# Kernel tuning notes

Measured on AMD Instinct MI355X. Metric: run time of the kernel, lower is better.

The kernel has to match this reference:

```python
import jax, jax.numpy as jnp
import numpy as np

BLOCK = 64
THRESH = 0.95
EPS = 1e-8


def setup_inputs() -> dict:
    key = jax.random.key(0)
    kq, kk, kv = jax.random.split(key, 3)
    S, D = 4096, 128
    q = jax.random.normal(kq, (S, D), dtype=jnp.float32)
    k = jax.random.normal(kk, (S, D), dtype=jnp.float32)
    v = jax.random.normal(kv, (S, D), dtype=jnp.float32)
    return {"q": q, "k": k, "v": v}


def reference(q, k, v):
    S, D = q.shape
    nb = S // BLOCK
    qb = q.reshape(nb, BLOCK, D)
    kb = k.reshape(nb, BLOCK, D)
    vb = v.reshape(nb, BLOCK, D)
    # all block-pair scores: [nb_q, nb_k, BLOCK_q, BLOCK_k]
    scores = jnp.einsum('ibd,jcd->ijbc', qb, kb)
    m = jnp.max(scores, axis=-1, keepdims=True)
    e = jnp.exp(scores - m)
    s = jnp.sum(e, axis=-1, keepdims=True)  # per-block-pair softmax denominator
    # top-p truncation mask: sort descending, cumsum, threshold
    srt = jnp.sort(e, axis=-1)[..., ::-1]
    cum = jnp.cumsum(srt, axis=-1)
    mask = cum < THRESH * s
    # NOTE: faithful to original — mask (in sorted order) is applied to the
    # UNSORTED exp_scores, exactly as the torch code does (indices unused).
    em = e * mask
    em = em / (jnp.sum(em, axis=-1, keepdims=True) + EPS)
    # accumulate over key blocks j (per-pair normalized weights, summed)
    out = jnp.einsum('ijbc,jcd->ibd', em, vb)
    return out.reshape(S, D)
```

## Files before the change

### kernel.cpp

```cpp
#include <hip/hip_runtime.h>
#include <cstdint>
#include <cstddef>


#define SEQ   4096
#define DIM   128
#define BLK   64
#define NB    (SEQ / BLK)
#define NJG   16
#define JPB   (NB / NJG)
#define NT    256
#define PSTR  12288
#define THRESH 0.95f
#define EPSF   1e-8f
#define PPART  (PSTR * NB)
#define PARTF  (NJG * SEQ * DIM)
#define WS_NEED ((size_t)PPART * 4 + (size_t)PARTF * 4)

typedef __attribute__((ext_vector_type(8))) _Float16 f16x8;
typedef __attribute__((ext_vector_type(4))) float    f32x4;

#define MFMAH(a, b, c) __builtin_amdgcn_mfma_f32_16x16x32_f16((a), (b), (c), 0, 0, 0)

union UH4 { uint2 u; _Float16 h[4]; };
union UH8 { uint4 u; f16x8 v; };

__device__ __forceinline__ void gll16(const uint* g, uint* l) {
  __builtin_amdgcn_global_load_lds(
      (const __attribute__((address_space(1))) void*)g,
      (__attribute__((address_space(3))) void*)l, 16, 0, 0);
}

__global__ __launch_bounds__(NT, 4) void eco_prep_kernel(
    const float* __restrict__ K, const float* __restrict__ V,
    uint* __restrict__ P, float* __restrict__ O) {
  const int tid = threadIdx.x;
  const int w   = blockIdx.x;
  const int jb  = w >> 4;
  const int sub = w & 15;

  if (tid < 128) {
    float4 z = {0.f, 0.f, 0.f, 0.f};
    ((float4*)O)[w * 128 + tid] = z;

    const float4* gk = (const float4*)(K + (size_t)jb * BLK * DIM);
    uint* dst = P + (size_t)jb * PSTR;
    int f = sub * 128 + tid;
    int r = f >> 5, c4 = f & 31;
    float4 x = gk[f];
    float xs[4] = {x.x, x.y, x.z, x.w};
    UH4 uh, ur;
#pragma unroll
    for (int e = 0; e < 4; ++e) {
      float v = xs[e];
      _Float16 h = (_Float16)v;
      uh.h[e] = h;
      ur.h[e] = (_Float16)(v - (float)h);
    }
    uint off = (uint)r * 64u + (((uint)(c4 >> 1) ^ (uint)(r & 15)) << 2) +
               (uint)((c4 & 1) << 1);
    *(uint2*)&dst[off]        = uh.u;
    *(uint2*)&dst[4096 + off] = ur.u;
  } else if (tid < 192) {
    const float* gv = V + (size_t)jb * BLK * DIM;
    uint4* dv = (uint4*)(P + (size_t)jb * PSTR + 8192);
    int idx = sub * 64 + (tid - 128);
    int ch = idx >> 7, d = idx & 127;
    UH8 u;
#pragma unroll
    for (int j = 0; j < 8; ++j)
      u.v[j] = (_Float16)gv[(ch * 8 + j) * DIM + d];
    dv[idx] = u.u;
  }
}

__global__ __launch_bounds__(NT) void eco_reduce_kernel(
    const float* __restrict__ Part, float* __restrict__ O) {
  const int gid = blockIdx.x * NT + threadIdx.x;
  const float4* p4 = (const float4*)Part;
  float4 a = p4[gid];
#pragma unroll
  for (int jg = 1; jg < NJG; ++jg) {
    float4 b = p4[(size_t)jg * (SEQ * DIM / 4) + gid];
    a.x += b.x; a.y += b.y; a.z += b.z; a.w += b.w;
  }
  ((float4*)O)[gid] = a;
}

template <bool PARTIAL>
__global__ __launch_bounds__(NT, 4) void eco_attn_kernel(
    const float* __restrict__ Q, const uint* __restrict__ P,
    float* __restrict__ O, float* __restrict__ Part) {
  __shared__ __align__(16) uint sK[8192];

  const int tid  = threadIdx.x;
  const int ib   = blockIdx.y;
  const int jg   = blockIdx.x;
  const int lane = tid & 63;
  const int wv   = tid >> 6;
  const int quad = lane >> 4;
  const int l16  = lane & 15;
  const int q4   = quad << 2;

  f16x8 qh[4], qr[4];
  {
    const float* qp = Q + (size_t)(ib * BLK + wv * 16 + l16) * DIM + quad * 8;
#pragma unroll
    for (int ks = 0; ks < 4; ++ks) {
      float4 x0 = *(const float4*)(qp + ks * 32);
      float4 x1 = *(const float4*)(qp + ks * 32 + 4);
      float xs[8] = {x0.x, x0.y, x0.z, x0.w, x1.x, x1.y, x1.z, x1.w};
      f16x8 h8, r8;
#pragma unroll
      for (int e = 0; e < 8; ++e) {
        float v = xs[e];
        _Float16 h = (_Float16)v;
        h8[e] = h;
        r8[e] = (_Float16)(v - (float)h);
      }
      qh[ks] = h8; qr[ks] = r8;
    }
  }

  const f32x4 zf = {0.f, 0.f, 0.f, 0.f};
  f32x4 pv[8];
#pragma unroll
  for (int i = 0; i < 8; ++i) pv[i] = zf;

  {
    const uint* gsrc = P + (size_t)(jg * JPB) * PSTR;
#pragma unroll
    for (int it = 0; it < 8; ++it) {
      int idx = (it * NT + tid) << 2;
      gll16(gsrc + idx, sK + idx);
    }
  }

  for (int jj = 0; jj < JPB; ++jj) {
    const int jb = jg * JPB + jj;
    __syncthreads();

    f32x4 acc[4];
#pragma unroll
    for (int nt = 0; nt < 4; ++nt) acc[nt] = zf;
#pragma unroll
    for (int nt = 0; nt < 4; ++nt) {
      const int rB = nt * 16 + l16;
      const uint rowoff = (uint)rB * 64u;
      const uint swk = (uint)(rB & 15);
#pragma unroll
      for (int ks = 0; ks < 4; ++ks) {
        uint off = rowoff + ((((uint)(ks * 4 + quad)) ^ swk) << 2);
        f16x8 bh = *(const f16x8*)&sK[off];
        f16x8 br = *(const f16x8*)&sK[4096 + off];
        acc[nt] = MFMAH(bh, qh[ks], acc[nt]);
        acc[nt] = MFMAH(br, qh[ks], acc[nt]);
        acc[nt] = MFMAH(bh, qr[ks], acc[nt]);
      }
    }
    __syncthreads();

    if (jj + 1 < JPB) {
      const uint* gsrc = P + (size_t)(jb + 1) * PSTR;
#pragma unroll
      for (int it = 0; it < 8; ++it) {
        int idx = (it * NT + tid) << 2;
        gll16(gsrc + idx, sK + idx);
      }
    }

    const uint* gvt = P + (size_t)jb * PSTR + 8192;

    bool doHi;
    uint2 u0, u1, u2, u3;

    {
      float a[16], e[16];
#pragma unroll
      for (int nt = 0; nt < 4; ++nt) {
#pragma unroll
        for (int rg = 0; rg < 4; ++rg) a[nt * 4 + rg] = acc[nt][rg];
      }
      float mt[8];
#pragma unroll
      for (int i = 0; i < 8; ++i) mt[i] = fmaxf(a[i], a[i + 8]);
#pragma unroll
      for (int w2 = 4; w2 >= 1; w2 >>= 1)
#pragma unroll
        for (int i = 0; i < w2; ++i) mt[i] = fmaxf(mt[i], mt[i + w2]);
      float m = mt[0];
      m = fmaxf(m, __shfl_xor(m, 16, 64));
      m = fmaxf(m, __shfl_xor(m, 32, 64));
#pragma unroll
      for (int i = 0; i < 16; ++i) { a[i] = __expf(a[i] - m); e[i] = a[i]; }
      float st[8];
#pragma unroll
      for (int i = 0; i < 8; ++i) st[i] = a[i] + a[i + 8];
#pragma unroll
      for (int w2 = 4; w2 >= 1; w2 >>= 1)
#pragma unroll
        for (int i = 0; i < w2; ++i) st[i] += st[i + w2];
      float sr = st[0];
      sr += __shfl_xor(sr, 16, 64);
      sr += __shfl_xor(sr, 32, 64);
      const float T = THRESH * sr;

      float cum = 1.0f;
      bool live = (cum < T);
      int t = live ? 1 : 0;
#pragma unroll
      for (int i = 0; i < 16; ++i) a[i] = (a[i] >= 1.0f) ? 0.f : a[i];
#pragma unroll
      for (int p4 = 0; p4 < 4; ++p4) {
        float M = fmaxf(fmaxf(fmaxf(a[0], a[1]), a[2]),
                        fmaxf(fmaxf(a[3], a[4]), a[5]));
        M = fmaxf(M, fmaxf(fmaxf(a[6],  a[7]),  a[8]));
        M = fmaxf(M, fmaxf(fmaxf(a[9],  a[10]), a[11]));
        M = fmaxf(M, fmaxf(fmaxf(a[12], a[13]), a[14]));
        M = fmaxf(M, a[15]);
        M = fmaxf(M, __shfl_xor(M, 16, 64));
        M = fmaxf(M, __shfl_xor(M, 32, 64));
        const float cn = cum + M;
        const bool cross = !(cn < T) || !(M > 0.f);
        if (live) { cum = cn; t += cross ? 0 : 1; }
        live = live && !cross;
#pragma unroll
        for (int i = 0; i < 16; ++i) a[i] = (a[i] >= M) ? 0.f : a[i];
      }

      while (__any(live)) {
        float M = fmaxf(fmaxf(fmaxf(a[0], a[1]), a[2]),
                        fmaxf(fmaxf(a[3], a[4]), a[5]));
        M = fmaxf(M, fmaxf(fmaxf(a[6],  a[7]),  a[8]));
        M = fmaxf(M, fmaxf(fmaxf(a[9],  a[10]), a[11]));
        M = fmaxf(M, fmaxf(fmaxf(a[12], a[13]), a[14]));
        M = fmaxf(M, a[15]);
        M = fmaxf(M, __shfl_xor(M, 16, 64));
        M = fmaxf(M, __shfl_xor(M, 32, 64));
        const float cn = cum + M;
        const bool cross = !(cn < T) || !(M > 0.f);
        if (live) { cum = cn; t += cross ? 0 : 1; }
        live = live && !cross;
#pragma unroll
        for (int i = 0; i < 16; ++i) a[i] = (a[i] >= M) ? 0.f : a[i];
      }

      {
        int tm = t;
        int o;
        o = __shfl_xor(tm, 1, 64); tm = (o > tm) ? o : tm;
        o = __shfl_xor(tm, 2, 64); tm = (o > tm) ? o : tm;
        o = __shfl_xor(tm, 4, 64); tm = (o > tm) ? o : tm;
        o = __shfl_xor(tm, 8, 64); tm = (o > tm) ? o : tm;
        doHi = (tm > 32);
      }

      float p = 0.f;
#pragma unroll
      for (int i = 0; i < 16; ++i) {
        int kidx = ((i >> 2) << 4) + q4 + (i & 3);
        p += (kidx < t) ? e[i] : 0.f;
      }
      p += __shfl_xor(p, 16, 64);
      p += __shfl_xor(p, 32, 64);
      const float rn = 1.0f / (p + EPSF);

      {
        UH4 z0, z1;
#pragma unroll
        for (int rg = 0; rg < 4; ++rg) {
          int k0 = q4 + rg;
          int k1 = 16 + q4 + rg;
          z0.h[rg] = (_Float16)((k0 < t) ? e[rg] * rn : 0.f);
          z1.h[rg] = (_Float16)((k1 < t) ? e[4 + rg] * rn : 0.f);
        }
        u0 = z0.u; u1 = z1.u;
      }
      if (doHi) {
        UH4 z2, z3;
#pragma unroll
        for (int rg = 0; rg < 4; ++rg) {
          int k2 = 32 + q4 + rg;
          int k3 = 48 + q4 + rg;
          z2.h[rg] = (_Float16)((k2 < t) ? e[8 + rg]  * rn : 0.f);
          z3.h[rg] = (_Float16)((k3 < t) ? e[12 + rg] * rn : 0.f);
        }
        u2 = z2.u; u3 = z3.u;
      }
    }

    const int sA  = ((quad & 1) << 5) + l16;
    const int sB  = sA + 16;
    const bool sel = ((quad >> 1) == 0);
    {
      int A0x = __shfl((int)u0.x, sA, 64);
      int A0y = __shfl((int)u0.y, sA, 64);
      int A1x = __shfl((int)u0.x, sB, 64);
      int A1y = __shfl((int)u0.y, sB, 64);
      int B0x = __shfl((int)u1.x, sA, 64);
      int B0y = __shfl((int)u1.y, sA, 64);
      int B1x = __shfl((int)u1.x, sB, 64);
      int B1y = __shfl((int)u1.y, sB, 64);
      UH8 w8;
      w8.u = make_uint4(sel ? (uint)A0x : (uint)B0x,
                        sel ? (uint)A0y : (uint)B0y,
                        sel ? (uint)A1x : (uint)B1x,
                        sel ? (uint)A1y : (uint)B1y);
      f16x8 wf0 = w8.v;
#pragma unroll
      for (int nt2 = 0; nt2 < 8; ++nt2) {
        f16x8 vf = *(const f16x8*)&gvt[((uint)(quad * 128 +
                                               nt2 * 16 + l16)) << 2];
        pv[nt2] = MFMAH(wf0, vf, pv[nt2]);
      }
    }
    if (doHi) {
      int A0x = __shfl((int)u2.x, sA, 64);
      int A0y = __shfl((int)u2.y, sA, 64);
      int A1x = __shfl((int)u2.x, sB, 64);
      int A1y = __shfl((int)u2.y, sB, 64);
      int B0x = __shfl((int)u3.x, sA, 64);
      int B0y = __shfl((int)u3.y, sA, 64);
      int B1x = __shfl((int)u3.x, sB, 64);
      int B1y = __shfl((int)u3.y, sB, 64);
      UH8 w8;
      w8.u = make_uint4(sel ? (uint)A0x : (uint)B0x,
                        sel ? (uint)A0y : (uint)B0y,
                        sel ? (uint)A1x : (uint)B1x,
                        sel ? (uint)A1y : (uint)B1y);
      f16x8 wf1 = w8.v;
#pragma unroll
      for (int nt2 = 0; nt2 < 8; ++nt2) {
        f16x8 vf = *(const f16x8*)&gvt[((uint)((4 + quad) * 128 +
                                               nt2 * 16 + l16)) << 2];
        pv[nt2] = MFMAH(wf1, vf, pv[nt2]);
      }
    }
  }

  if constexpr (PARTIAL) {
    float* pb = Part + (size_t)jg * (SEQ * DIM);
    const int row0 = ib * BLK + wv * 16 + quad * 4;
#pragma unroll
    for (int nt2 = 0; nt2 < 8; ++nt2) {
      const int col = nt2 * 16 + l16;
#pragma unroll
      for (int rg = 0; rg < 4; ++rg)
        pb[(size_t)(row0 + rg) * DIM + col] = pv[nt2][rg];
    }
  } else {
#pragma unroll
    for (int nt2 = 0; nt2 < 8; ++nt2) {
      const int col  = nt2 * 16 + l16;
      const int row0 = ib * BLK + wv * 16 + quad * 4;
#pragma unroll
      for (int rg = 0; rg < 4; ++rg)
        atomicAdd(O + (size_t)(row0 + rg) * DIM + col, pv[nt2][rg]);
    }
  }
}

extern "C" void kernel_launch(void* const* d_in, const int* in_sizes, int n_in,
                              void* d_out, int out_size, void* d_ws, size_t ws_size,
                              hipStream_t stream) {
  (void)in_sizes; (void)n_in; (void)out_size;
  const float* q = (const float*)d_in[0];
  const float* k = (const float*)d_in[1];
  const float* v = (const float*)d_in[2];
  float* out = (float*)d_out;
  uint* prep = (uint*)d_ws;
  float* part = (float*)((char*)d_ws + (size_t)PPART * 4);

  eco_prep_kernel<<<dim3(NB * 16), dim3(NT), 0, stream>>>(k, v, prep, out);
  if (ws_size >= WS_NEED) {
    eco_attn_kernel<true><<<dim3(NJG, NB), dim3(NT), 0, stream>>>(q, prep, out, part);
    eco_reduce_kernel<<<dim3(SEQ * DIM / 4 / NT), dim3(NT), 0, stream>>>(part, out);
  } else {
    eco_attn_kernel<false><<<dim3(NJG, NB), dim3(NT), 0, stream>>>(q, prep, out, nullptr);
  }
}
```

Before: 99.74 us.

## Read K tiles directly from global memory instead of staging through LDS

Removes the LDS buffer and the global_load_lds double-buffered prefetch of K hi/lo tiles, so each wave now loads its MFMA B operands straight from global (L2/L1-cached) memory. The prep kernel stops swizzling K to match. Barriers are gone and occupancy bounds change from 4 to 3 blocks per SM. The doHi reduction is replaced with a wave-wide __any over all lanes instead of a 16-lane max shuffle. The aim is to drop barrier and LDS traffic, at the cost of redundant global loads across the four waves and higher load latency with no prefetch overlap.

```diff
diff --git a/kernel.cpp b/kernel.cpp
--- a/kernel.cpp
+++ b/kernel.cpp
@@ -25,12 +25,6 @@
 union UH4 { uint2 u; _Float16 h[4]; };
 union UH8 { uint4 u; f16x8 v; };
 
-__device__ __forceinline__ void gll16(const uint* g, uint* l) {
-  __builtin_amdgcn_global_load_lds(
-      (const __attribute__((address_space(1))) void*)g,
-      (__attribute__((address_space(3))) void*)l, 16, 0, 0);
-}
-
 __global__ __launch_bounds__(NT, 4) void eco_prep_kernel(
     const float* __restrict__ K, const float* __restrict__ V,
     uint* __restrict__ P, float* __restrict__ O) {
@@ -57,8 +51,7 @@
       uh.h[e] = h;
       ur.h[e] = (_Float16)(v - (float)h);
     }
-    uint off = (uint)r * 64u + (((uint)(c4 >> 1) ^ (uint)(r & 15)) << 2) +
-               (uint)((c4 & 1) << 1);
+    uint off = (uint)r * 64u + (uint)c4 * 2u;
     *(uint2*)&dst[off]        = uh.u;
     *(uint2*)&dst[4096 + off] = ur.u;
   } else if (tid < 192) {
@@ -88,11 +81,9 @@
 }
 
 template <bool PARTIAL>
-__global__ __launch_bounds__(NT, 4) void eco_attn_kernel(
+__global__ __launch_bounds__(NT, 3) void eco_attn_kernel(
     const float* __restrict__ Q, const uint* __restrict__ P,
     float* __restrict__ O, float* __restrict__ Part) {
-  __shared__ __align__(16) uint sK[8192];
-
   const int tid  = threadIdx.x;
   const int ib   = blockIdx.y;
   const int jg   = blockIdx.x;
@@ -127,18 +118,10 @@
 #pragma unroll
   for (int i = 0; i < 8; ++i) pv[i] = zf;
 
-  {
-    const uint* gsrc = P + (size_t)(jg * JPB) * PSTR;
-#pragma unroll
-    for (int it = 0; it < 8; ++it) {
-      int idx = (it * NT + tid) << 2;
-      gll16(gsrc + idx, sK + idx);
-    }
-  }
-
   for (int jj = 0; jj < JPB; ++jj) {
     const int jb = jg * JPB + jj;
-    __syncthreads();
+    const uint* gk  = P + (size_t)jb * PSTR;
+    const uint* gvt = gk + 8192;
 
     f32x4 acc[4];
 #pragma unroll
@@ -147,29 +130,16 @@
     for (int nt = 0; nt < 4; ++nt) {
       const int rB = nt * 16 + l16;
       const uint rowoff = (uint)rB * 64u;
-      const uint swk = (uint)(rB & 15);
 #pragma unroll
       for (int ks = 0; ks < 4; ++ks) {
-        uint off = rowoff + ((((uint)(ks * 4 + quad)) ^ swk) << 2);
-        f16x8 bh = *(const f16x8*)&sK[off];
-        f16x8 br = *(const f16x8*)&sK[4096 + off];
+        uint off = rowoff + (uint)((ks * 4 + quad) << 2);
+        f16x8 bh = *(const f16x8*)&gk[off];
+        f16x8 br = *(const f16x8*)&gk[4096 + off];
         acc[nt] = MFMAH(bh, qh[ks], acc[nt]);
         acc[nt] = MFMAH(br, qh[ks], acc[nt]);
         acc[nt] = MFMAH(bh, qr[ks], acc[nt]);
       }
     }
-    __syncthreads();
-
-    if (jj + 1 < JPB) {
-      const uint* gsrc = P + (size_t)(jb + 1) * PSTR;
-#pragma unroll
-      for (int it = 0; it < 8; ++it) {
-        int idx = (it * NT + tid) << 2;
-        gll16(gsrc + idx, sK + idx);
-      }
-    }
-
-    const uint* gvt = P + (size_t)jb * PSTR + 8192;
 
     bool doHi;
     uint2 u0, u1, u2, u3;
@@ -245,15 +215,7 @@
         for (int i = 0; i < 16; ++i) a[i] = (a[i] >= M) ? 0.f : a[i];
       }
 
-      {
-        int tm = t;
-        int o;
-        o = __shfl_xor(tm, 1, 64); tm = (o > tm) ? o : tm;
-        o = __shfl_xor(tm, 2, 64); tm = (o > tm) ? o : tm;
-        o = __shfl_xor(tm, 4, 64); tm = (o > tm) ? o : tm;
-        o = __shfl_xor(tm, 8, 64); tm = (o > tm) ? o : tm;
-        doHi = (tm > 32);
-      }
+      doHi = __any(t > 32);
 
       float p = 0.f;
 #pragma unroll
```

After: 145.0 us. 45.4% more time.

## Permute K rows in prep so softmax weights land in MFMA A-operand layout

Applied to the files above, without the earlier changes.

The prep kernel now stores K rows in a permuted order, so each lane's score accumulator values line up directly with the f16x8 A-operand layout the PV MFMA needs. This removes the 16 cross-lane shuffles and selects per block pair that previously rearranged the weights. The max-reduction shuffle chain for doHi becomes a single wave vote. Zeroing of the output in prep is skipped when the partial-sum path is used, since the reduce kernel overwrites it. Correctness depends on the index mapping for the threshold mask and for the V ordering staying consistent with the permuted key order.

```diff
diff --git a/kernel.cpp b/kernel.cpp
--- a/kernel.cpp
+++ b/kernel.cpp
@@ -31,6 +31,7 @@
       (__attribute__((address_space(3))) void*)l, 16, 0, 0);
 }
 
+template <bool ZERO>
 __global__ __launch_bounds__(NT, 4) void eco_prep_kernel(
     const float* __restrict__ K, const float* __restrict__ V,
     uint* __restrict__ P, float* __restrict__ O) {
@@ -40,14 +41,18 @@
   const int sub = w & 15;
 
   if (tid < 128) {
-    float4 z = {0.f, 0.f, 0.f, 0.f};
-    ((float4*)O)[w * 128 + tid] = z;
+    if constexpr (ZERO) {
+      float4 z = {0.f, 0.f, 0.f, 0.f};
+      ((float4*)O)[w * 128 + tid] = z;
+    }
 
     const float4* gk = (const float4*)(K + (size_t)jb * BLK * DIM);
     uint* dst = P + (size_t)jb * PSTR;
     int f = sub * 128 + tid;
     int r = f >> 5, c4 = f & 31;
-    float4 x = gk[f];
+    int nt = r >> 4, q = (r >> 2) & 3, rg = r & 3;
+    int pi = (q << 3) | ((nt & 1) << 5) | ((nt >> 1) << 2) | rg;
+    float4 x = gk[pi * 32 + c4];
     float xs[4] = {x.x, x.y, x.z, x.w};
     UH4 uh, ur;
 #pragma unroll
@@ -100,7 +105,7 @@
   const int wv   = tid >> 6;
   const int quad = lane >> 4;
   const int l16  = lane & 15;
-  const int q4   = quad << 2;
+  const int q8   = quad << 3;
 
   f16x8 qh[4], qr[4];
   {
@@ -172,7 +177,7 @@
     const uint* gvt = P + (size_t)jb * PSTR + 8192;
 
     bool doHi;
-    uint2 u0, u1, u2, u3;
+    f16x8 wf0, wf1;
 
     {
       float a[16], e[16];
@@ -245,20 +250,12 @@
         for (int i = 0; i < 16; ++i) a[i] = (a[i] >= M) ? 0.f : a[i];
       }
 
-      {
-        int tm = t;
-        int o;
-        o = __shfl_xor(tm, 1, 64); tm = (o > tm) ? o : tm;
-        o = __shfl_xor(tm, 2, 64); tm = (o > tm) ? o : tm;
-        o = __shfl_xor(tm, 4, 64); tm = (o > tm) ? o : tm;
-        o = __shfl_xor(tm, 8, 64); tm = (o > tm) ? o : tm;
-        doHi = (tm > 32);
-      }
+      doHi = __any(t > 32);
 
       float p = 0.f;
 #pragma unroll
       for (int i = 0; i < 16; ++i) {
-        int kidx = ((i >> 2) << 4) + q4 + (i & 3);
+        int kidx = q8 + (((i >> 2) & 1) << 5) + ((i >> 3) << 2) + (i & 3);
         p += (kidx < t) ? e[i] : 0.f;
       }
       p += __shfl_xor(p, 16, 64);
@@ -266,47 +263,28 @@
       const float rn = 1.0f / (p + EPSF);
 
       {
-        UH4 z0, z1;
-#pragma unroll
-        for (int rg = 0; rg < 4; ++rg) {
-          int k0 = q4 + rg;
-          int k1 = 16 + q4 + rg;
-          z0.h[rg] = (_Float16)((k0 < t) ? e[rg] * rn : 0.f);
-          z1.h[rg] = (_Float16)((k1 < t) ? e[4 + rg] * rn : 0.f);
+        UH8 w0;
+#pragma unroll
+        for (int j = 0; j < 8; ++j) {
+          int i0 = ((j >> 2) << 3) + (j & 3);
+          int k0 = q8 + j;
+          w0.v[j] = (_Float16)((k0 < t) ? e[i0] * rn : 0.f);
         }
-        u0 = z0.u; u1 = z1.u;
+        wf0 = w0.v;
       }
       if (doHi) {
-        UH4 z2, z3;
-#pragma unroll
-        for (int rg = 0; rg < 4; ++rg) {
-          int k2 = 32 + q4 + rg;
-          int k3 = 48 + q4 + rg;
-          z2.h[rg] = (_Float16)((k2 < t) ? e[8 + rg]  * rn : 0.f);
-          z3.h[rg] = (_Float16)((k3 < t) ? e[12 + rg] * rn : 0.f);
+        UH8 w1;
+#pragma unroll
+        for (int j = 0; j < 8; ++j) {
+          int i1 = 4 + ((j >> 2) << 3) + (j & 3);
+          int k1 = q8 + 32 + j;
+          w1.v[j] = (_Float16)((k1 < t) ? e[i1] * rn : 0.f);
         }
-        u2 = z2.u; u3 = z3.u;
-      }
-    }
-
-    const int sA  = ((quad & 1) << 5) + l16;
-    const int sB  = sA + 16;
-    const bool sel = ((quad >> 1) == 0);
+        wf1 = w1.v;
+      }
+    }
+
     {
-      int A0x = __shfl((int)u0.x, sA, 64);
-      int A0y = __shfl((int)u0.y, sA, 64);
-      int A1x = __shfl((int)u0.x, sB, 64);
-      int A1y = __shfl((int)u0.y, sB, 64);
-      int B0x = __shfl((int)u1.x, sA, 64);
-      int B0y = __shfl((int)u1.y, sA, 64);
-      int B1x = __shfl((int)u1.x, sB, 64);
-      int B1y = __shfl((int)u1.y, sB, 64);
-      UH8 w8;
-      w8.u = make_uint4(sel ? (uint)A0x : (uint)B0x,
-                        sel ? (uint)A0y : (uint)B0y,
-                        sel ? (uint)A1x : (uint)B1x,
-                        sel ? (uint)A1y : (uint)B1y);
-      f16x8 wf0 = w8.v;
 #pragma unroll
       for (int nt2 = 0; nt2 < 8; ++nt2) {
         f16x8 vf = *(const f16x8*)&gvt[((uint)(quad * 128 +
@@ -315,20 +293,6 @@
       }
     }
     if (doHi) {
-      int A0x = __shfl((int)u2.x, sA, 64);
-      int A0y = __shfl((int)u2.y, sA, 64);
-      int A1x = __shfl((int)u2.x, sB, 64);
-      int A1y = __shfl((int)u2.y, sB, 64);
-      int B0x = __shfl((int)u3.x, sA, 64);
-      int B0y = __shfl((int)u3.y, sA, 64);
-      int B1x = __shfl((int)u3.x, sB, 64);
-      int B1y = __shfl((int)u3.y, sB, 64);
-      UH8 w8;
-      w8.u = make_uint4(sel ? (uint)A0x : (uint)B0x,
-                        sel ? (uint)A0y : (uint)B0y,
-                        sel ? (uint)A1x : (uint)B1x,
-                        sel ? (uint)A1y : (uint)B1y);
-      f16x8 wf1 = w8.v;
 #pragma unroll
       for (int nt2 = 0; nt2 < 8; ++nt2) {
         f16x8 vf = *(const f16x8*)&gvt[((uint)((4 + quad) * 128 +
@@ -371,11 +335,12 @@
   uint* prep = (uint*)d_ws;
   float* part = (float*)((char*)d_ws + (size_t)PPART * 4);
 
-  eco_prep_kernel<<<dim3(NB * 16), dim3(NT), 0, stream>>>(k, v, prep, out);
   if (ws_size >= WS_NEED) {
+    eco_prep_kernel<false><<<dim3(NB * 16), dim3(NT), 0, stream>>>(k, v, prep, out);
     eco_attn_kernel<true><<<dim3(NJG, NB), dim3(NT), 0, stream>>>(q, prep, out, part);
     eco_reduce_kernel<<<dim3(SEQ * DIM / 4 / NT), dim3(NT), 0, stream>>>(part, out);
   } else {
+    eco_prep_kernel<true><<<dim3(NB * 16), dim3(NT), 0, stream>>>(k, v, prep, out);
     eco_attn_kernel<false><<<dim3(NJG, NB), dim3(NT), 0, stream>>>(q, prep, out, nullptr);
   }
 }
```

New measurement: 98.04 us (median of 2 runs). Within noise of the previous version (-1.7%).
